# Optimization experiments

Measured on AMD Instinct MI355X. Metric: run time of the kernel, lower is better.

## Reference

```python
import jax, jax.numpy as jnp
import numpy as np

DIM = 512
N_HEADS = 8
HEAD_DIM = DIM // N_HEADS


def setup_inputs() -> dict:
    key = jax.random.key(0)
    ks = jax.random.split(key, 11)
    B, S = 2, 2048
    s = 1.0 / np.sqrt(DIM)
    return {
        "q": jax.random.normal(ks[0], (B, S, DIM), jnp.float32),
        "k": jax.random.normal(ks[1], (B, S, DIM), jnp.float32),
        "v": jax.random.normal(ks[2], (B, S, DIM), jnp.float32),
        "Wq": jax.random.normal(ks[3], (DIM, DIM), jnp.float32) * s,
        "bq": jnp.zeros((DIM,), jnp.float32),
        "Wk": jax.random.normal(ks[4], (DIM, DIM), jnp.float32) * s,
        "bk": jnp.zeros((DIM,), jnp.float32),
        "Wv": jax.random.normal(ks[5], (DIM, DIM), jnp.float32) * s,
        "bv": jnp.zeros((DIM,), jnp.float32),
        "Wo": jax.random.normal(ks[6], (DIM, DIM), jnp.float32) * s,
        "bo": jnp.zeros((DIM,), jnp.float32),
    }


def reference(q, k, v, Wq, bq, Wk, bk, Wv, bv, Wo, bo):
    B, S, _ = q.shape
    # projections; split into heads: [B, H, S, Dh]
    def proj(x, W, b):
        y = x @ W.T + b
        return y.reshape(B, -1, N_HEADS, HEAD_DIM).transpose(0, 2, 1, 3)

    qh = proj(q, Wq, bq)
    kh = proj(k, Wk, bk)
    vh = proj(v, Wv, bv)
    scores = jnp.einsum("bhsd,bhtd->bhst", qh, kh) / np.sqrt(HEAD_DIM)
    attn = jax.nn.softmax(scores, axis=-1)  # dropout = identity in eval
    ctx = jnp.einsum("bhst,bhtd->bhsd", attn, vh)
    ctx = ctx.transpose(0, 2, 1, 3).reshape(B, S, DIM)
    out = ctx @ Wo.T + bo
    return out, attn
```

## Files before the change

kernel.cpp:

```cpp
#include <hip/hip_runtime.h>
#include <math.h>

#define DIM 512
#define NH 8
#define HD 64
#define SS 2048
#define NB 2

typedef __bf16 bf16;
typedef __attribute__((ext_vector_type(8))) __bf16 bf16x8;
typedef __attribute__((ext_vector_type(4))) float f32x4;

__device__ inline bf16x8 cvt8(const float* s) {
  bf16x8 o;
#pragma unroll
  for (int i = 0; i < 8; ++i) o[i] = (bf16)s[i];
  return o;
}

__global__ __launch_bounds__(256) void qkv_proj_kernel(
    const float* __restrict__ xq, const float* __restrict__ xk, const float* __restrict__ xv,
    const float* __restrict__ Wq, const float* __restrict__ bq,
    const float* __restrict__ Wk, const float* __restrict__ bk,
    const float* __restrict__ Wv, const float* __restrict__ bv,
    bf16* __restrict__ qh, bf16* __restrict__ kh, bf16* __restrict__ vh)
{
  const int which = blockIdx.z;
  const float* A    = (which == 0) ? xq : (which == 1) ? xk : xv;
  const float* W    = (which == 0) ? Wq : (which == 1) ? Wk : Wv;
  const float* bias = (which == 0) ? bq : (which == 1) ? bk : bv;
  bf16* out         = (which == 0) ? qh : (which == 1) ? kh : vh;
  const float oscale = (which == 0) ? 0.125f : 1.0f;

  __shared__ bf16 As[128][72];
  __shared__ bf16 Bs[64][72];

  const int m0 = blockIdx.x * 128;
  const int n0 = blockIdx.y * 64;
  const int tid = threadIdx.x;
  const int w = tid >> 6, l = tid & 63;
  const int l16 = l & 15, lg = l >> 4;
  const int wm = w >> 1, wn = w & 1;

  f32x4 acc[4][2];
#pragma unroll
  for (int mf = 0; mf < 4; ++mf)
#pragma unroll
    for (int nf = 0; nf < 2; ++nf) acc[mf][nf] = (f32x4){0.f, 0.f, 0.f, 0.f};

  for (int k0 = 0; k0 < DIM; k0 += 64) {
    __syncthreads();
    {
      const int r = tid >> 1, hf = (tid & 1) * 32;
      const float* src = &A[(size_t)(m0 + r) * DIM + k0 + hf];
      bf16* dst = &As[r][hf];
#pragma unroll
      for (int i = 0; i < 4; ++i) ((bf16x8*)dst)[i] = cvt8(src + i * 8);
    }
    if (tid < 128) {
      const int r = tid >> 1, hf = (tid & 1) * 32;
      const float* src = &W[(size_t)(n0 + r) * DIM + k0 + hf];
      bf16* dst = &Bs[r][hf];
#pragma unroll
      for (int i = 0; i < 4; ++i) ((bf16x8*)dst)[i] = cvt8(src + i * 8);
    }
    __syncthreads();

#pragma unroll
    for (int kk = 0; kk < 2; ++kk) {
      bf16x8 bfr[2];
      bfr[0] = *(const bf16x8*)&Bs[wn * 32 + l16][kk * 32 + lg * 8];
      bfr[1] = *(const bf16x8*)&Bs[wn * 32 + 16 + l16][kk * 32 + lg * 8];
#pragma unroll
      for (int mf = 0; mf < 4; ++mf) {
        const bf16x8 af = *(const bf16x8*)&As[wm * 64 + mf * 16 + l16][kk * 32 + lg * 8];
        acc[mf][0] = __builtin_amdgcn_mfma_f32_16x16x32_bf16(af, bfr[0], acc[mf][0], 0, 0, 0);
        acc[mf][1] = __builtin_amdgcn_mfma_f32_16x16x32_bf16(af, bfr[1], acc[mf][1], 0, 0, 0);
      }
    }
  }

  const int h = blockIdx.y;
#pragma unroll
  for (int mf = 0; mf < 4; ++mf) {
#pragma unroll
    for (int nf = 0; nf < 2; ++nf) {
      const int d = wn * 32 + nf * 16 + l16;
#pragma unroll
      for (int ri = 0; ri < 4; ++ri) {
        const int row = m0 + wm * 64 + mf * 16 + lg * 4 + ri;
        const int b = row >> 11, s = row & 2047;
        out[((size_t)(b * NH + h) * SS + s) * HD + d] =
            (bf16)((acc[mf][nf][ri] + bias[n0 + d]) * oscale);
      }
    }
  }
}

__global__ __launch_bounds__(256) void attn_kernel(
    const bf16* __restrict__ qh, const bf16* __restrict__ kh, const bf16* __restrict__ vh,
    float* __restrict__ attn, bf16* __restrict__ ctx)
{
  __shared__ bf16 Ks[128][72];
  __shared__ bf16 Vt[64][136];
  __shared__ bf16 Ps[4][16][136];

  const int bh = blockIdx.y;
  const int q0 = blockIdx.x * 64;
  const int tid = threadIdx.x;
  const int w   = tid >> 6;
  const int l   = tid & 63;
  const int l16 = l & 15;
  const int lg  = l >> 4;

  const bf16* qp = qh + (size_t)bh * SS * HD;
  const bf16* kp = kh + (size_t)bh * SS * HD;
  const bf16* vp = vh + (size_t)bh * SS * HD;

  const int qrow = q0 + w * 16 + l16;
  const bf16x8 qf0 = *(const bf16x8*)&qp[(size_t)qrow * HD + lg * 8];
  const bf16x8 qf1 = *(const bf16x8*)&qp[(size_t)qrow * HD + 32 + lg * 8];

  float m_run[4], l_run[4];
#pragma unroll
  for (int r = 0; r < 4; ++r) { m_run[r] = -1e30f; l_run[r] = 0.f; }

  for (int t0 = 0; t0 < SS; t0 += 128) {
    __syncthreads();
    {
      const int r = tid >> 1, hh = tid & 1;
      const bf16* src = &kp[(size_t)(t0 + r) * HD + hh * 32];
      bf16* dst = &Ks[r][hh * 32];
#pragma unroll
      for (int i = 0; i < 4; ++i) ((bf16x8*)dst)[i] = ((const bf16x8*)src)[i];
    }
    __syncthreads();

    f32x4 accS[8];
#pragma unroll
    for (int n = 0; n < 8; ++n) {
      const bf16x8 kf0 = *(const bf16x8*)&Ks[n * 16 + l16][lg * 8];
      const bf16x8 kf1 = *(const bf16x8*)&Ks[n * 16 + l16][32 + lg * 8];
      f32x4 acc = {0.f, 0.f, 0.f, 0.f};
      acc = __builtin_amdgcn_mfma_f32_16x16x32_bf16(qf0, kf0, acc, 0, 0, 0);
      acc = __builtin_amdgcn_mfma_f32_16x16x32_bf16(qf1, kf1, acc, 0, 0, 0);
      accS[n] = acc;
    }
#pragma unroll
    for (int r = 0; r < 4; ++r) {
      float tmax = accS[0][r];
#pragma unroll
      for (int n = 1; n < 8; ++n) tmax = fmaxf(tmax, accS[n][r]);
      const float nm = fmaxf(m_run[r], tmax);
      float sum = 0.f;
#pragma unroll
      for (int n = 0; n < 8; ++n) sum += __expf(accS[n][r] - nm);
      l_run[r] = l_run[r] * __expf(m_run[r] - nm) + sum;
      m_run[r] = nm;
    }
  }

#pragma unroll
  for (int r = 0; r < 4; ++r) {
    float m = m_run[r], ls = l_run[r];
#pragma unroll
    for (int off = 1; off < 16; off <<= 1) {
      const float m2 = __shfl_xor(m, off);
      const float l2 = __shfl_xor(ls, off);
      const float nm = fmaxf(m, m2);
      ls = ls * __expf(m - nm) + l2 * __expf(m2 - nm);
      m = nm;
    }
    m_run[r] = m;
    l_run[r] = 1.f / ls;
  }

  f32x4 accC[4];
#pragma unroll
  for (int dt = 0; dt < 4; ++dt) accC[dt] = (f32x4){0.f, 0.f, 0.f, 0.f};

  float* arow_base = attn + ((size_t)(bh * SS + q0 + w * 16)) * SS;

  for (int t0 = 0; t0 < SS; t0 += 128) {
    __syncthreads();
    if (tid < 128) {
      const int r = tid;
      bf16 vrow[64];
      const bf16* src = &vp[(size_t)(t0 + r) * HD];
#pragma unroll
      for (int i = 0; i < 8; ++i) ((bf16x8*)vrow)[i] = ((const bf16x8*)src)[i];
#pragma unroll
      for (int d = 0; d < 64; ++d) Vt[d][r] = vrow[d];
    } else {
      const int r = tid - 128;
      const bf16* src = &kp[(size_t)(t0 + r) * HD];
      bf16* dst = &Ks[r][0];
#pragma unroll
      for (int i = 0; i < 8; ++i) ((bf16x8*)dst)[i] = ((const bf16x8*)src)[i];
    }
    __syncthreads();

    f32x4 accS[8];
#pragma unroll
    for (int n = 0; n < 8; ++n) {
      const bf16x8 kf0 = *(const bf16x8*)&Ks[n * 16 + l16][lg * 8];
      const bf16x8 kf1 = *(const bf16x8*)&Ks[n * 16 + l16][32 + lg * 8];
      f32x4 acc = {0.f, 0.f, 0.f, 0.f};
      acc = __builtin_amdgcn_mfma_f32_16x16x32_bf16(qf0, kf0, acc, 0, 0, 0);
      acc = __builtin_amdgcn_mfma_f32_16x16x32_bf16(qf1, kf1, acc, 0, 0, 0);
      accS[n] = acc;
    }

#pragma unroll
    for (int n = 0; n < 8; ++n) {
#pragma unroll
      for (int r = 0; r < 4; ++r) {
        const int row = lg * 4 + r;
        const float p = __expf(accS[n][r] - m_run[r]) * l_run[r];
        arow_base[(size_t)row * SS + t0 + n * 16 + l16] = p;
        Ps[w][row][n * 16 + l16] = (bf16)p;
      }
    }

#pragma unroll
    for (int ts = 0; ts < 4; ++ts) {
      const bf16x8 pa = *(const bf16x8*)&Ps[w][l16][ts * 32 + lg * 8];
#pragma unroll
      for (int dt = 0; dt < 4; ++dt) {
        const bf16x8 vb = *(const bf16x8*)&Vt[dt * 16 + l16][ts * 32 + lg * 8];
        accC[dt] = __builtin_amdgcn_mfma_f32_16x16x32_bf16(pa, vb, accC[dt], 0, 0, 0);
      }
    }
  }

  const int b = bh >> 3, h = bh & 7;
#pragma unroll
  for (int dt = 0; dt < 4; ++dt)
#pragma unroll
    for (int r = 0; r < 4; ++r) {
      const int s = q0 + w * 16 + lg * 4 + r;
      ctx[((size_t)b * SS + s) * DIM + h * HD + dt * 16 + l16] = (bf16)accC[dt][r];
    }
}

__global__ __launch_bounds__(256) void out_proj_kernel(
    const bf16* __restrict__ ctx, const float* __restrict__ Wo, const float* __restrict__ bo,
    float* __restrict__ out)
{
  __shared__ bf16 As[128][72];
  __shared__ bf16 Bs[64][72];

  const int m0 = blockIdx.x * 128;
  const int n0 = blockIdx.y * 64;
  const int tid = threadIdx.x;
  const int w = tid >> 6, l = tid & 63;
  const int l16 = l & 15, lg = l >> 4;
  const int wm = w >> 1, wn = w & 1;

  f32x4 acc[4][2];
#pragma unroll
  for (int mf = 0; mf < 4; ++mf)
#pragma unroll
    for (int nf = 0; nf < 2; ++nf) acc[mf][nf] = (f32x4){0.f, 0.f, 0.f, 0.f};

  for (int k0 = 0; k0 < DIM; k0 += 64) {
    __syncthreads();
    {
      const int r = tid >> 1, hf = (tid & 1) * 32;
      const bf16* src = &ctx[(size_t)(m0 + r) * DIM + k0 + hf];
      bf16* dst = &As[r][hf];
#pragma unroll
      for (int i = 0; i < 4; ++i) ((bf16x8*)dst)[i] = ((const bf16x8*)src)[i];
    }
    if (tid < 128) {
      const int r = tid >> 1, hf = (tid & 1) * 32;
      const float* src = &Wo[(size_t)(n0 + r) * DIM + k0 + hf];
      bf16* dst = &Bs[r][hf];
#pragma unroll
      for (int i = 0; i < 4; ++i) ((bf16x8*)dst)[i] = cvt8(src + i * 8);
    }
    __syncthreads();

#pragma unroll
    for (int kk = 0; kk < 2; ++kk) {
      bf16x8 bfr[2];
      bfr[0] = *(const bf16x8*)&Bs[wn * 32 + l16][kk * 32 + lg * 8];
      bfr[1] = *(const bf16x8*)&Bs[wn * 32 + 16 + l16][kk * 32 + lg * 8];
#pragma unroll
      for (int mf = 0; mf < 4; ++mf) {
        const bf16x8 af = *(const bf16x8*)&As[wm * 64 + mf * 16 + l16][kk * 32 + lg * 8];
        acc[mf][0] = __builtin_amdgcn_mfma_f32_16x16x32_bf16(af, bfr[0], acc[mf][0], 0, 0, 0);
        acc[mf][1] = __builtin_amdgcn_mfma_f32_16x16x32_bf16(af, bfr[1], acc[mf][1], 0, 0, 0);
      }
    }
  }

#pragma unroll
  for (int mf = 0; mf < 4; ++mf) {
#pragma unroll
    for (int nf = 0; nf < 2; ++nf) {
      const int c = n0 + wn * 32 + nf * 16 + l16;
#pragma unroll
      for (int ri = 0; ri < 4; ++ri) {
        const int row = m0 + wm * 64 + mf * 16 + lg * 4 + ri;
        out[(size_t)row * DIM + c] = acc[mf][nf][ri] + bo[c];
      }
    }
  }
}

extern "C" void kernel_launch(void* const* d_in, const int* in_sizes, int n_in,
                              void* d_out, int out_size, void* d_ws, size_t ws_size,
                              hipStream_t stream) {
  const float* q  = (const float*)d_in[0];
  const float* k  = (const float*)d_in[1];
  const float* v  = (const float*)d_in[2];
  const float* Wq = (const float*)d_in[3];
  const float* bq = (const float*)d_in[4];
  const float* Wk = (const float*)d_in[5];
  const float* bk = (const float*)d_in[6];
  const float* Wv = (const float*)d_in[7];
  const float* bv = (const float*)d_in[8];
  const float* Wo = (const float*)d_in[9];
  const float* bo = (const float*)d_in[10];

  float* out0 = (float*)d_out;
  float* attn = out0 + (size_t)NB * SS * DIM;

  const size_t HSZ = (size_t)NB * NH * SS * HD;
  bf16* qh  = (bf16*)d_ws;
  bf16* kh  = qh + HSZ;
  bf16* vh  = kh + HSZ;
  bf16* ctx = vh + HSZ;

  dim3 g1(NB * SS / 128, DIM / 64, 3);
  qkv_proj_kernel<<<g1, 256, 0, stream>>>(q, k, v, Wq, bq, Wk, bk, Wv, bv, qh, kh, vh);

  dim3 g2(SS / 64, NB * NH);
  attn_kernel<<<g2, 256, 0, stream>>>(qh, kh, vh, attn, ctx);

  dim3 g3(NB * SS / 128, DIM / 64);
  out_proj_kernel<<<g3, 256, 0, stream>>>(ctx, Wo, bo, out0);
}
```

Measured before the change: 148.6 us.

## Prefetch next tiles into registers and swizzle V transpose in shared memory

```diff
diff --git a/kernel.cpp b/kernel.cpp
--- a/kernel.cpp
+++ b/kernel.cpp
@@ -41,6 +41,7 @@
   const int w = tid >> 6, l = tid & 63;
   const int l16 = l & 15, lg = l >> 4;
   const int wm = w >> 1, wn = w & 1;
+  const int r = tid >> 1, hf = (tid & 1) * 32;
 
   f32x4 acc[4][2];
 #pragma unroll
@@ -48,24 +49,39 @@
 #pragma unroll
     for (int nf = 0; nf < 2; ++nf) acc[mf][nf] = (f32x4){0.f, 0.f, 0.f, 0.f};
 
+  bf16x8 aPre[4], bPre[4];
+  {
+    const float* srcA = &A[(size_t)(m0 + r) * DIM + hf];
+#pragma unroll
+    for (int i = 0; i < 4; ++i) aPre[i] = cvt8(srcA + i * 8);
+    if (tid < 128) {
+      const float* srcB = &W[(size_t)(n0 + r) * DIM + hf];
+#pragma unroll
+      for (int i = 0; i < 4; ++i) bPre[i] = cvt8(srcB + i * 8);
+    }
+    bf16* dstA = &As[r][hf];
+#pragma unroll
+    for (int i = 0; i < 4; ++i) ((bf16x8*)dstA)[i] = aPre[i];
+    if (tid < 128) {
+      bf16* dstB = &Bs[r][hf];
+#pragma unroll
+      for (int i = 0; i < 4; ++i) ((bf16x8*)dstB)[i] = bPre[i];
+    }
+  }
+  __syncthreads();
+
   for (int k0 = 0; k0 < DIM; k0 += 64) {
-    __syncthreads();
-    {
-      const int r = tid >> 1, hf = (tid & 1) * 32;
-      const float* src = &A[(size_t)(m0 + r) * DIM + k0 + hf];
-      bf16* dst = &As[r][hf];
-#pragma unroll
-      for (int i = 0; i < 4; ++i) ((bf16x8*)dst)[i] = cvt8(src + i * 8);
-    }
-    if (tid < 128) {
-      const int r = tid >> 1, hf = (tid & 1) * 32;
-      const float* src = &W[(size_t)(n0 + r) * DIM + k0 + hf];
-      bf16* dst = &Bs[r][hf];
-#pragma unroll
-      for (int i = 0; i < 4; ++i) ((bf16x8*)dst)[i] = cvt8(src + i * 8);
-    }
-    __syncthreads();
-
+    const int kn = k0 + 64;
+    if (kn < DIM) {
+      const float* srcA = &A[(size_t)(m0 + r) * DIM + kn + hf];
+#pragma unroll
+      for (int i = 0; i < 4; ++i) aPre[i] = cvt8(srcA + i * 8);
+      if (tid < 128) {
+        const float* srcB = &W[(size_t)(n0 + r) * DIM + kn + hf];
+#pragma unroll
+        for (int i = 0; i < 4; ++i) bPre[i] = cvt8(srcB + i * 8);
+      }
+    }
 #pragma unroll
     for (int kk = 0; kk < 2; ++kk) {
       bf16x8 bfr[2];
@@ -78,6 +94,18 @@
         acc[mf][1] = __builtin_amdgcn_mfma_f32_16x16x32_bf16(af, bfr[1], acc[mf][1], 0, 0, 0);
       }
     }
+    __syncthreads();
+    if (kn < DIM) {
+      bf16* dstA = &As[r][hf];
+#pragma unroll
+      for (int i = 0; i < 4; ++i) ((bf16x8*)dstA)[i] = aPre[i];
+      if (tid < 128) {
+        bf16* dstB = &Bs[r][hf];
+#pragma unroll
+        for (int i = 0; i < 4; ++i) ((bf16x8*)dstB)[i] = bPre[i];
+      }
+    }
+    __syncthreads();
   }
 
   const int h = blockIdx.y;
@@ -102,7 +130,7 @@
     float* __restrict__ attn, bf16* __restrict__ ctx)
 {
   __shared__ bf16 Ks[128][72];
-  __shared__ bf16 Vt[64][136];
+  __shared__ bf16 Vt[64 * 128];
   __shared__ bf16 Ps[4][16][136];
 
   const int bh = blockIdx.y;
@@ -123,46 +151,60 @@
 
   float m_run[4], l_run[4];
 #pragma unroll
-  for (int r = 0; r < 4; ++r) { m_run[r] = -1e30f; l_run[r] = 0.f; }
-
+  for (int rr = 0; rr < 4; ++rr) { m_run[rr] = -1e30f; l_run[rr] = 0.f; }
+
+  const int r2 = tid >> 1, hh = (tid & 1) * 32;
+  {
+    const bf16* src = &kp[(size_t)r2 * HD + hh];
+    bf16* dst = &Ks[r2][hh];
+#pragma unroll
+    for (int i = 0; i < 4; ++i) ((bf16x8*)dst)[i] = ((const bf16x8*)src)[i];
+  }
+  __syncthreads();
+
+  bf16x8 kPre[4];
   for (int t0 = 0; t0 < SS; t0 += 128) {
-    __syncthreads();
-    {
-      const int r = tid >> 1, hh = tid & 1;
-      const bf16* src = &kp[(size_t)(t0 + r) * HD + hh * 32];
-      bf16* dst = &Ks[r][hh * 32];
-#pragma unroll
-      for (int i = 0; i < 4; ++i) ((bf16x8*)dst)[i] = ((const bf16x8*)src)[i];
-    }
-    __syncthreads();
+    const int tn = t0 + 128;
+    if (tn < SS) {
+      const bf16* src = &kp[(size_t)(tn + r2) * HD + hh];
+#pragma unroll
+      for (int i = 0; i < 4; ++i) kPre[i] = ((const bf16x8*)src)[i];
+    }
 
     f32x4 accS[8];
 #pragma unroll
     for (int n = 0; n < 8; ++n) {
       const bf16x8 kf0 = *(const bf16x8*)&Ks[n * 16 + l16][lg * 8];
       const bf16x8 kf1 = *(const bf16x8*)&Ks[n * 16 + l16][32 + lg * 8];
-      f32x4 acc = {0.f, 0.f, 0.f, 0.f};
-      acc = __builtin_amdgcn_mfma_f32_16x16x32_bf16(qf0, kf0, acc, 0, 0, 0);
-      acc = __builtin_amdgcn_mfma_f32_16x16x32_bf16(qf1, kf1, acc, 0, 0, 0);
-      accS[n] = acc;
-    }
-#pragma unroll
-    for (int r = 0; r < 4; ++r) {
-      float tmax = accS[0][r];
-#pragma unroll
-      for (int n = 1; n < 8; ++n) tmax = fmaxf(tmax, accS[n][r]);
-      const float nm = fmaxf(m_run[r], tmax);
+      f32x4 a = {0.f, 0.f, 0.f, 0.f};
+      a = __builtin_amdgcn_mfma_f32_16x16x32_bf16(qf0, kf0, a, 0, 0, 0);
+      a = __builtin_amdgcn_mfma_f32_16x16x32_bf16(qf1, kf1, a, 0, 0, 0);
+      accS[n] = a;
+    }
+#pragma unroll
+    for (int rr = 0; rr < 4; ++rr) {
+      float tmax = accS[0][rr];
+#pragma unroll
+      for (int n = 1; n < 8; ++n) tmax = fmaxf(tmax, accS[n][rr]);
+      const float nm = fmaxf(m_run[rr], tmax);
       float sum = 0.f;
 #pragma unroll
-      for (int n = 0; n < 8; ++n) sum += __expf(accS[n][r] - nm);
-      l_run[r] = l_run[r] * __expf(m_run[r] - nm) + sum;
-      m_run[r] = nm;
-    }
-  }
-
-#pragma unroll
-  for (int r = 0; r < 4; ++r) {
-    float m = m_run[r], ls = l_run[r];
+      for (int n = 0; n < 8; ++n) sum += __expf(accS[n][rr] - nm);
+      l_run[rr] = l_run[rr] * __expf(m_run[rr] - nm) + sum;
+      m_run[rr] = nm;
+    }
+    __syncthreads();
+    if (tn < SS) {
+      bf16* dst = &Ks[r2][hh];
+#pragma unroll
+      for (int i = 0; i < 4; ++i) ((bf16x8*)dst)[i] = kPre[i];
+    }
+    __syncthreads();
+  }
+
+#pragma unroll
+  for (int rr = 0; rr < 4; ++rr) {
+    float m = m_run[rr], ls = l_run[rr];
 #pragma unroll
     for (int off = 1; off < 16; off <<= 1) {
       const float m2 = __shfl_xor(m, off);
@@ -171,8 +213,8 @@
       ls = ls * __expf(m - nm) + l2 * __expf(m2 - nm);
       m = nm;
     }
-    m_run[r] = m;
-    l_run[r] = 1.f / ls;
+    m_run[rr] = m;
+    l_run[rr] = 1.f / ls;
   }
 
   f32x4 accC[4];
@@ -181,43 +223,66 @@
 
   float* arow_base = attn + ((size_t)(bh * SS + q0 + w * 16)) * SS;
 
+  const bool isV = (tid < 128);
+  const int vdb = (tid & 127) >> 4;
+  const int vtb = tid & 15;
+  const int kr  = tid & 127;
+
+  {
+    if (isV) {
+      bf16x8 vr[8];
+#pragma unroll
+      for (int i = 0; i < 8; ++i)
+        vr[i] = *(const bf16x8*)&vp[(size_t)(vtb * 8 + i) * HD + vdb * 8];
+#pragma unroll
+      for (int j = 0; j < 8; ++j) {
+        bf16x8 o;
+#pragma unroll
+        for (int i = 0; i < 8; ++i) o[i] = vr[i][j];
+        *(bf16x8*)&Vt[(vdb * 8 + j) * 128 + ((vtb ^ j) << 3)] = o;
+      }
+    } else {
+      const bf16* src = &kp[(size_t)kr * HD];
+      bf16* dst = &Ks[kr][0];
+#pragma unroll
+      for (int i = 0; i < 8; ++i) ((bf16x8*)dst)[i] = ((const bf16x8*)src)[i];
+    }
+  }
+  __syncthreads();
+
+  bf16x8 pre[8];
   for (int t0 = 0; t0 < SS; t0 += 128) {
-    __syncthreads();
-    if (tid < 128) {
-      const int r = tid;
-      bf16 vrow[64];
-      const bf16* src = &vp[(size_t)(t0 + r) * HD];
-#pragma unroll
-      for (int i = 0; i < 8; ++i) ((bf16x8*)vrow)[i] = ((const bf16x8*)src)[i];
-#pragma unroll
-      for (int d = 0; d < 64; ++d) Vt[d][r] = vrow[d];
-    } else {
-      const int r = tid - 128;
-      const bf16* src = &kp[(size_t)(t0 + r) * HD];
-      bf16* dst = &Ks[r][0];
-#pragma unroll
-      for (int i = 0; i < 8; ++i) ((bf16x8*)dst)[i] = ((const bf16x8*)src)[i];
-    }
-    __syncthreads();
+    const int tn = t0 + 128;
+    if (tn < SS) {
+      if (isV) {
+#pragma unroll
+        for (int i = 0; i < 8; ++i)
+          pre[i] = *(const bf16x8*)&vp[(size_t)(tn + vtb * 8 + i) * HD + vdb * 8];
+      } else {
+        const bf16* src = &kp[(size_t)(tn + kr) * HD];
+#pragma unroll
+        for (int i = 0; i < 8; ++i) pre[i] = ((const bf16x8*)src)[i];
+      }
+    }
 
     f32x4 accS[8];
 #pragma unroll
     for (int n = 0; n < 8; ++n) {
       const bf16x8 kf0 = *(const bf16x8*)&Ks[n * 16 + l16][lg * 8];
       const bf16x8 kf1 = *(const bf16x8*)&Ks[n * 16 + l16][32 + lg * 8];
-      f32x4 acc = {0.f, 0.f, 0.f, 0.f};
-      acc = __builtin_amdgcn_mfma_f32_16x16x32_bf16(qf0, kf0, acc, 0, 0, 0);
-      acc = __builtin_amdgcn_mfma_f32_16x16x32_bf16(qf1, kf1, acc, 0, 0, 0);
-      accS[n] = acc;
+      f32x4 a = {0.f, 0.f, 0.f, 0.f};
+      a = __builtin_amdgcn_mfma_f32_16x16x32_bf16(qf0, kf0, a, 0, 0, 0);
+      a = __builtin_amdgcn_mfma_f32_16x16x32_bf16(qf1, kf1, a, 0, 0, 0);
+      accS[n] = a;
     }
 
 #pragma unroll
     for (int n = 0; n < 8; ++n) {
 #pragma unroll
-      for (int r = 0; r < 4; ++r) {
-        const int row = lg * 4 + r;
-        const float p = __expf(accS[n][r] - m_run[r]) * l_run[r];
-        arow_base[(size_t)row * SS + t0 + n * 16 + l16] = p;
+      for (int rr = 0; rr < 4; ++rr) {
+        const int row = lg * 4 + rr;
+        const float p = __expf(accS[n][rr] - m_run[rr]) * l_run[rr];
+        __builtin_nontemporal_store(p, &arow_base[(size_t)row * SS + t0 + n * 16 + l16]);
         Ps[w][row][n * 16 + l16] = (bf16)p;
       }
     }
@@ -227,19 +292,37 @@
       const bf16x8 pa = *(const bf16x8*)&Ps[w][l16][ts * 32 + lg * 8];
 #pragma unroll
       for (int dt = 0; dt < 4; ++dt) {
-        const bf16x8 vb = *(const bf16x8*)&Vt[dt * 16 + l16][ts * 32 + lg * 8];
+        const int d = dt * 16 + l16;
+        const bf16x8 vb = *(const bf16x8*)&Vt[d * 128 + (((ts * 4 + lg) ^ (l16 & 7)) << 3)];
         accC[dt] = __builtin_amdgcn_mfma_f32_16x16x32_bf16(pa, vb, accC[dt], 0, 0, 0);
       }
     }
+    __syncthreads();
+    if (tn < SS) {
+      if (isV) {
+#pragma unroll
+        for (int j = 0; j < 8; ++j) {
+          bf16x8 o;
+#pragma unroll
+          for (int i = 0; i < 8; ++i) o[i] = pre[i][j];
+          *(bf16x8*)&Vt[(vdb * 8 + j) * 128 + ((vtb ^ j) << 3)] = o;
+        }
+      } else {
+        bf16* dst = &Ks[kr][0];
+#pragma unroll
+        for (int i = 0; i < 8; ++i) ((bf16x8*)dst)[i] = pre[i];
+      }
+    }
+    __syncthreads();
   }
 
   const int b = bh >> 3, h = bh & 7;
 #pragma unroll
   for (int dt = 0; dt < 4; ++dt)
 #pragma unroll
-    for (int r = 0; r < 4; ++r) {
-      const int s = q0 + w * 16 + lg * 4 + r;
-      ctx[((size_t)b * SS + s) * DIM + h * HD + dt * 16 + l16] = (bf16)accC[dt][r];
+    for (int rr = 0; rr < 4; ++rr) {
+      const int s = q0 + w * 16 + lg * 4 + rr;
+      ctx[((size_t)b * SS + s) * DIM + h * HD + dt * 16 + l16] = (bf16)accC[dt][rr];
     }
 }
 
@@ -256,6 +339,7 @@
   const int w = tid >> 6, l = tid & 63;
   const int l16 = l & 15, lg = l >> 4;
   const int wm = w >> 1, wn = w & 1;
+  const int r = tid >> 1, hf = (tid & 1) * 32;
 
   f32x4 acc[4][2];
 #pragma unroll
@@ -263,24 +347,39 @@
 #pragma unroll
     for (int nf = 0; nf < 2; ++nf) acc[mf][nf] = (f32x4){0.f, 0.f, 0.f, 0.f};
 
+  bf16x8 aPre[4], bPre[4];
+  {
+    const bf16* srcA = &ctx[(size_t)(m0 + r) * DIM + hf];
+#pragma unroll
+    for (int i = 0; i < 4; ++i) aPre[i] = ((const bf16x8*)srcA)[i];
+    if (tid < 128) {
+      const float* srcB = &Wo[(size_t)(n0 + r) * DIM + hf];
+#pragma unroll
+      for (int i = 0; i < 4; ++i) bPre[i] = cvt8(srcB + i * 8);
+    }
+    bf16* dstA = &As[r][hf];
+#pragma unroll
+    for (int i = 0; i < 4; ++i) ((bf16x8*)dstA)[i] = aPre[i];
+    if (tid < 128) {
+      bf16* dstB = &Bs[r][hf];
+#pragma unroll
+      for (int i = 0; i < 4; ++i) ((bf16x8*)dstB)[i] = bPre[i];
+    }
+  }
+  __syncthreads();
+
   for (int k0 = 0; k0 < DIM; k0 += 64) {
-    __syncthreads();
-    {
-      const int r = tid >> 1, hf = (tid & 1) * 32;
-      const bf16* src = &ctx[(size_t)(m0 + r) * DIM + k0 + hf];
-      bf16* dst = &As[r][hf];
-#pragma unroll
-      for (int i = 0; i < 4; ++i) ((bf16x8*)dst)[i] = ((const bf16x8*)src)[i];
-    }
-    if (tid < 128) {
-      const int r = tid >> 1, hf = (tid & 1) * 32;
-      const float* src = &Wo[(size_t)(n0 + r) * DIM + k0 + hf];
-      bf16* dst = &Bs[r][hf];
-#pragma unroll
-      for (int i = 0; i < 4; ++i) ((bf16x8*)dst)[i] = cvt8(src + i * 8);
-    }
-    __syncthreads();
-
+    const int kn = k0 + 64;
+    if (kn < DIM) {
+      const bf16* srcA = &ctx[(size_t)(m0 + r) * DIM + kn + hf];
+#pragma unroll
+      for (int i = 0; i < 4; ++i) aPre[i] = ((const bf16x8*)srcA)[i];
+      if (tid < 128) {
+        const float* srcB = &Wo[(size_t)(n0 + r) * DIM + kn + hf];
+#pragma unroll
+        for (int i = 0; i < 4; ++i) bPre[i] = cvt8(srcB + i * 8);
+      }
+    }
 #pragma unroll
     for (int kk = 0; kk < 2; ++kk) {
       bf16x8 bfr[2];
@@ -293,6 +392,18 @@
         acc[mf][1] = __builtin_amdgcn_mfma_f32_16x16x32_bf16(af, bfr[1], acc[mf][1], 0, 0, 0);
       }
     }
+    __syncthreads();
+    if (kn < DIM) {
+      bf16* dstA = &As[r][hf];
+#pragma unroll
+      for (int i = 0; i < 4; ++i) ((bf16x8*)dstA)[i] = aPre[i];
+      if (tid < 128) {
+        bf16* dstB = &Bs[r][hf];
+#pragma unroll
+        for (int i = 0; i < 4; ++i) ((bf16x8*)dstB)[i] = bPre[i];
+      }
+    }
+    __syncthreads();
   }
 
 #pragma unroll
```

Measured after the change: 176.2 us. +18.6%, slower.
